# Performance work log

Hardware: AMD Instinct MI355X
Metric: run time of the kernel (lower is better)

## Reference

```python
import jax, jax.numpy as jnp
import numpy as np

N_PTS = 2048
NUM_GABOR = 2
IMG_H = 512
IMG_W = 512
CHUNK = 32  # gaussians per scan step
ALPHA_THRESH = 1.0 / 255.0


def setup_inputs() -> dict:
    key = jax.random.key(0)
    ks = jax.random.split(key, 6)
    xyz = jax.random.uniform(ks[0], (N_PTS, 2), dtype=jnp.float32) * jnp.array([IMG_W, IMG_H], jnp.float32)
    cov2d = jax.random.uniform(ks[1], (N_PTS, 3), dtype=jnp.float32)
    features_dc = jax.random.normal(ks[2], (N_PTS, 3), dtype=jnp.float32)
    opacity = jnp.ones((N_PTS, 1), jnp.float32)
    gabor_freqs = (jax.random.uniform(ks[3], (N_PTS * NUM_GABOR, 2), dtype=jnp.float32) - 0.5) * 0.002
    gabor_weights = jax.random.uniform(ks[4], (N_PTS * NUM_GABOR, 1), dtype=jnp.float32) * -5.0
    background = jnp.ones((3,), jnp.float32)
    return dict(xyz=xyz, cov2d=cov2d, features_dc=features_dc, opacity=opacity,
                gabor_freqs=gabor_freqs, gabor_weights=gabor_weights,
                background=background, H=IMG_H, W=IMG_W)


def _render(xyz, cov2d, features_dc, opacity, gabor_freqs, gabor_weights, H, W):
    n = xyz.shape[0]
    g = gabor_freqs.shape[0] // n
    dt = xyz.dtype
    # cov elements with lower bound (SLV=False branch)
    covs = cov2d + jnp.array([0.5, 0.0, 0.5], dt)
    sxx, sxy, syy = covs[:, 0], covs[:, 1], covs[:, 2]
    det = sxx * syy - sxy * sxy
    valid = det > 1e-8
    det_s = jnp.where(valid, det, 1.0)
    conic_a = syy / det_s
    conic_b = -sxy / det_s
    conic_c = sxx / det_s
    # radius from max eigenvalue (for visibility filter / radii output)
    mid = 0.5 * (sxx + syy)
    lam = mid + jnp.sqrt(jnp.maximum(mid * mid - det, 0.1))
    radii = jnp.where(valid, jnp.ceil(3.0 * jnp.sqrt(lam)), 0.0).astype(jnp.int32)

    colors = jax.nn.sigmoid(features_dc)                      # color_norm=True
    freqs = jnp.exp(gabor_freqs).reshape(n, g, 2)             # get_gabor_freqs
    gw = jax.nn.sigmoid(gabor_weights).reshape(n, g)          # get_gabor_weights

    px = (jnp.arange(W, dtype=dt) + 0.5)[None, :]             # (1, W)
    py = (jnp.arange(H, dtype=dt) + 0.5)[:, None]             # (H, 1)

    steps = n // CHUNK
    def chunked(a):
        return a.reshape((steps, CHUNK) + a.shape[1:])

    xs = (chunked(xyz[:, 0]), chunked(xyz[:, 1]),
          chunked(conic_a), chunked(conic_b), chunked(conic_c),
          chunked(opacity[:, 0]), chunked(colors),
          chunked(freqs[:, :, 0]), chunked(freqs[:, :, 1]),
          chunked(gw), chunked(valid))

    def body(acc, args):
        x, y, ca, cb, cc, op, col, fx, fy, w, vm = args
        dx = px[None, :, :] - x[:, None, None]                 # (C,1,W)
        dy = py[None, :, :] - y[:, None, None]                 # (C,H,1)
        sigma = 0.5 * (ca[:, None, None] * dx * dx + cc[:, None, None] * dy * dy) \
                + cb[:, None, None] * (dx * dy)                # (C,H,W)
        alpha = op[:, None, None] * jnp.exp(-sigma)
        alpha = jnp.minimum(alpha, 0.999)
        alpha = jnp.where((alpha < ALPHA_THRESH) | (~vm[:, None, None]), 0.0, alpha)
        # gabor modulation: 1 + sum_k w_k * cos(fx_k*dx + fy_k*dy)
        arg = fx[:, :, None, None] * dx[:, None, :, :] + fy[:, :, None, None] * dy[:, None, :, :]
        mod = 1.0 + jnp.sum(w[:, :, None, None] * jnp.cos(arg), axis=1)  # (C,H,W)
        wgt = alpha * mod
        acc = acc + jnp.einsum('nhw,nc->hwc', wgt, col)
        return acc, None

    out, _ = jax.lax.scan(body, jnp.zeros((H, W, 3), dt), xs)
    img = jnp.clip(out, 0.0, 1.0)                              # (H,W,3)
    render = jnp.transpose(img[None], (0, 3, 1, 2))            # (1,3,H,W)
    return render, radii


def reference(xyz, cov2d, features_dc, opacity, gabor_freqs, gabor_weights, background, H, W):
    render, radii = _render(xyz, cov2d, features_dc, opacity, gabor_freqs, gabor_weights, H, W)
    visibility = radii > 0
    return render, radii, visibility
```

## Files before the change

### kernel.cpp

```cpp
#include <hip/hip_runtime.h>
#include <math.h>

#define NPTS 2048
#define NG 2
#define IMG_H 512
#define IMG_W 512
#define HW (IMG_H * IMG_W)
#define RENDER_SIZE (3 * HW)
#define S_MAX 5.5412636f

__device__ __forceinline__ float sigmoidf_(float x) {
    return 1.0f / (1.0f + expf(-x));
}

__global__ void init_kernel(const float* __restrict__ cov2d, float* __restrict__ out) {
    int i = blockIdx.x * blockDim.x + threadIdx.x;
    if (i < RENDER_SIZE) out[i] = 0.0f;
    if (i < NPTS) {
        float sxx = cov2d[i * 3 + 0] + 0.5f;
        float sxy = cov2d[i * 3 + 1];
        float syy = cov2d[i * 3 + 2] + 0.5f;
        float det = __fsub_rn(__fmul_rn(sxx, syy), __fmul_rn(sxy, sxy));
        bool valid = det > 1e-8f;
        float mid = __fmul_rn(0.5f, __fadd_rn(sxx, syy));
        float t = __fsub_rn(__fmul_rn(mid, mid), det);
        t = fmaxf(t, 0.1f);
        float lam = __fadd_rn(mid, sqrtf(t));
        float r = valid ? ceilf(__fmul_rn(3.0f, sqrtf(lam))) : 0.0f;
        out[RENDER_SIZE + i] = r;
        out[RENDER_SIZE + NPTS + i] = (r > 0.0f) ? 1.0f : 0.0f;
    }
}

__global__ __launch_bounds__(64) void splat_kernel(
    const float* __restrict__ xyz, const float* __restrict__ cov2d,
    const float* __restrict__ fdc, const float* __restrict__ opac,
    const float* __restrict__ gfreq, const float* __restrict__ gwts,
    float* __restrict__ out)
{
    int p = blockIdx.x;
    float sxx = cov2d[p * 3 + 0] + 0.5f;
    float sxy = cov2d[p * 3 + 1];
    float syy = cov2d[p * 3 + 2] + 0.5f;
    float det = sxx * syy - sxy * sxy;
    if (!(det > 1e-8f)) return;

    float inv = 1.0f / det;
    float ca = syy * inv;
    float cb = -sxy * inv;
    float cc = sxx * inv;

    float xn = xyz[p * 2 + 0];
    float yn = xyz[p * 2 + 1];
    float op = opac[p];

    float c0 = sigmoidf_(fdc[p * 3 + 0]);
    float c1 = sigmoidf_(fdc[p * 3 + 1]);
    float c2 = sigmoidf_(fdc[p * 3 + 2]);

    float fx0 = expf(gfreq[(p * NG + 0) * 2 + 0]);
    float fy0 = expf(gfreq[(p * NG + 0) * 2 + 1]);
    float fx1 = expf(gfreq[(p * NG + 1) * 2 + 0]);
    float fy1 = expf(gfreq[(p * NG + 1) * 2 + 1]);
    float w0 = sigmoidf_(gwts[p * NG + 0]);
    float w1 = sigmoidf_(gwts[p * NG + 1]);

    float dxm = sqrtf(2.0f * S_MAX * sxx) + 0.01f;
    float dym = sqrtf(2.0f * S_MAX * syy) + 0.01f;
    int x0 = max(0, (int)ceilf(xn - dxm - 0.5f));
    int x1 = min(IMG_W - 1, (int)floorf(xn + dxm - 0.5f));
    int y0 = max(0, (int)ceilf(yn - dym - 0.5f));
    int y1 = min(IMG_H - 1, (int)floorf(yn + dym - 0.5f));
    int bw = x1 - x0 + 1;
    int bh = y1 - y0 + 1;
    if (bw <= 0 || bh <= 0) return;
    int area = bw * bh;

    for (int idx = threadIdx.x; idx < area; idx += 64) {
        int ix = x0 + idx % bw;
        int iy = y0 + idx / bw;
        float dx = (ix + 0.5f) - xn;
        float dy = (iy + 0.5f) - yn;
        float sigma = 0.5f * (ca * dx * dx + cc * dy * dy) + cb * (dx * dy);
        float alpha = op * expf(-sigma);
        alpha = fminf(alpha, 0.999f);
        if (alpha < (1.0f / 255.0f)) continue;
        float mod = 1.0f + w0 * cosf(fx0 * dx + fy0 * dy)
                         + w1 * cosf(fx1 * dx + fy1 * dy);
        float wgt = alpha * mod;
        int pix = iy * IMG_W + ix;
        atomicAdd(&out[pix],          wgt * c0);
        atomicAdd(&out[HW + pix],     wgt * c1);
        atomicAdd(&out[2 * HW + pix], wgt * c2);
    }
}

__global__ void clamp_kernel(float* __restrict__ out) {
    int i = blockIdx.x * blockDim.x + threadIdx.x;
    if (i < RENDER_SIZE) {
        float v = out[i];
        out[i] = fminf(fmaxf(v, 0.0f), 1.0f);
    }
}

extern "C" void kernel_launch(void* const* d_in, const int* in_sizes, int n_in,
                              void* d_out, int out_size, void* d_ws, size_t ws_size,
                              hipStream_t stream) {
    const float* xyz   = (const float*)d_in[0];
    const float* cov2d = (const float*)d_in[1];
    const float* fdc   = (const float*)d_in[2];
    const float* opac  = (const float*)d_in[3];
    const float* gfreq = (const float*)d_in[4];
    const float* gwts  = (const float*)d_in[5];
    float* out = (float*)d_out;

    int blocks = (RENDER_SIZE + 255) / 256;
    init_kernel<<<blocks, 256, 0, stream>>>(cov2d, out);
    splat_kernel<<<NPTS, 64, 0, stream>>>(xyz, cov2d, fdc, opac, gfreq, gwts, out);
    clamp_kernel<<<blocks, 256, 0, stream>>>(out);
}
```

Baseline: 79.59 us.

## Replace atomic splatting with per-tile gather rendering in a single fused kernel

Replaces the three-kernel pipeline (zero/radii init, per-gaussian atomic scatter, clamp) with one kernel that assigns each 32x8 pixel tile to a block. Each block culls all gaussians against its tile's bounds, stages the parameters of the overlapping ones in shared memory, accumulates color per pixel in registers, then clamps and writes once. The radii and visibility outputs are computed by two threads per block. This removes global atomics, the separate zero and clamp passes, and the extra launches. In exchange every block scans the full gaussian list, and tiles with more than 128 overlapping gaussians would silently drop the excess.

Result: no change. 79.11 us (-0.6%).

```diff
diff --git a/kernel.cpp b/kernel.cpp
--- a/kernel.cpp
+++ b/kernel.cpp
@@ -9,14 +9,43 @@
 #define RENDER_SIZE (3 * HW)
 #define S_MAX 5.5412636f
 
+#define TILE_W 32
+#define TILE_H 8
+#define TILES_X (IMG_W / TILE_W)
+#define TILES_Y (IMG_H / TILE_H)
+#define NTILES (TILES_X * TILES_Y)
+#define NTHREADS 256
+#define CAP 128
+
 __device__ __forceinline__ float sigmoidf_(float x) {
     return 1.0f / (1.0f + expf(-x));
 }
 
-__global__ void init_kernel(const float* __restrict__ cov2d, float* __restrict__ out) {
-    int i = blockIdx.x * blockDim.x + threadIdx.x;
-    if (i < RENDER_SIZE) out[i] = 0.0f;
-    if (i < NPTS) {
+struct PParam {
+    float xn, yn, ca, cb, cc, op;
+    float c0, c1, c2;
+    float fx0, fy0, fx1, fy1, w0, w1, pad;
+};
+
+__global__ __launch_bounds__(NTHREADS) void render_kernel(
+    const float* __restrict__ xyz, const float* __restrict__ cov2d,
+    const float* __restrict__ fdc, const float* __restrict__ opac,
+    const float* __restrict__ gfreq, const float* __restrict__ gwts,
+    float* __restrict__ out)
+{
+    __shared__ int s_cnt;
+    __shared__ int s_idx[CAP];
+    __shared__ PParam s_prm[CAP];
+
+    const int tid = threadIdx.x;
+    const int tile = blockIdx.x;
+    const int x0 = (tile % TILES_X) * TILE_W;
+    const int y0 = (tile / TILES_X) * TILE_H;
+
+    if (tid == 0) s_cnt = 0;
+
+    if (tid < 2) {
+        int i = tile * 2 + tid;
         float sxx = cov2d[i * 3 + 0] + 0.5f;
         float sxy = cov2d[i * 3 + 1];
         float syy = cov2d[i * 3 + 2] + 0.5f;
@@ -30,77 +59,79 @@
         out[RENDER_SIZE + i] = r;
         out[RENDER_SIZE + NPTS + i] = (r > 0.0f) ? 1.0f : 0.0f;
     }
-}
+    __syncthreads();
 
-__global__ __launch_bounds__(64) void splat_kernel(
-    const float* __restrict__ xyz, const float* __restrict__ cov2d,
-    const float* __restrict__ fdc, const float* __restrict__ opac,
-    const float* __restrict__ gfreq, const float* __restrict__ gwts,
-    float* __restrict__ out)
-{
-    int p = blockIdx.x;
-    float sxx = cov2d[p * 3 + 0] + 0.5f;
-    float sxy = cov2d[p * 3 + 1];
-    float syy = cov2d[p * 3 + 2] + 0.5f;
-    float det = sxx * syy - sxy * sxy;
-    if (!(det > 1e-8f)) return;
+    const float txlo = x0 + 0.5f, txhi = x0 + (TILE_W - 1) + 0.5f;
+    const float tylo = y0 + 0.5f, tyhi = y0 + (TILE_H - 1) + 0.5f;
+    for (int p = tid; p < NPTS; p += NTHREADS) {
+        float2 c = ((const float2*)xyz)[p];
+        float sxx = cov2d[p * 3 + 0] + 0.5f;
+        float sxy = cov2d[p * 3 + 1];
+        float syy = cov2d[p * 3 + 2] + 0.5f;
+        float det = sxx * syy - sxy * sxy;
+        if (!(det > 1e-8f)) continue;
+        float dxn = fmaxf(0.0f, fmaxf(txlo - c.x, c.x - txhi));
+        float dyn = fmaxf(0.0f, fmaxf(tylo - c.y, c.y - tyhi));
+        if (dxn * dxn <= 2.0f * S_MAX * sxx + 0.25f &&
+            dyn * dyn <= 2.0f * S_MAX * syy + 0.25f) {
+            int slot = atomicAdd(&s_cnt, 1);
+            if (slot < CAP) s_idx[slot] = p;
+        }
+    }
+    __syncthreads();
+    const int n = min(s_cnt, CAP);
 
-    float inv = 1.0f / det;
-    float ca = syy * inv;
-    float cb = -sxy * inv;
-    float cc = sxx * inv;
+    for (int i = tid; i < n; i += NTHREADS) {
+        int p = s_idx[i];
+        float sxx = cov2d[p * 3 + 0] + 0.5f;
+        float sxy = cov2d[p * 3 + 1];
+        float syy = cov2d[p * 3 + 2] + 0.5f;
+        float inv = 1.0f / (sxx * syy - sxy * sxy);
+        PParam q;
+        q.xn = xyz[p * 2 + 0];
+        q.yn = xyz[p * 2 + 1];
+        q.ca = syy * inv;
+        q.cb = -sxy * inv;
+        q.cc = sxx * inv;
+        q.op = opac[p];
+        q.c0 = sigmoidf_(fdc[p * 3 + 0]);
+        q.c1 = sigmoidf_(fdc[p * 3 + 1]);
+        q.c2 = sigmoidf_(fdc[p * 3 + 2]);
+        q.fx0 = expf(gfreq[(p * NG + 0) * 2 + 0]);
+        q.fy0 = expf(gfreq[(p * NG + 0) * 2 + 1]);
+        q.fx1 = expf(gfreq[(p * NG + 1) * 2 + 0]);
+        q.fy1 = expf(gfreq[(p * NG + 1) * 2 + 1]);
+        q.w0 = sigmoidf_(gwts[p * NG + 0]);
+        q.w1 = sigmoidf_(gwts[p * NG + 1]);
+        q.pad = 0.0f;
+        s_prm[i] = q;
+    }
+    __syncthreads();
 
-    float xn = xyz[p * 2 + 0];
-    float yn = xyz[p * 2 + 1];
-    float op = opac[p];
-
-    float c0 = sigmoidf_(fdc[p * 3 + 0]);
-    float c1 = sigmoidf_(fdc[p * 3 + 1]);
-    float c2 = sigmoidf_(fdc[p * 3 + 2]);
-
-    float fx0 = expf(gfreq[(p * NG + 0) * 2 + 0]);
-    float fy0 = expf(gfreq[(p * NG + 0) * 2 + 1]);
-    float fx1 = expf(gfreq[(p * NG + 1) * 2 + 0]);
-    float fy1 = expf(gfreq[(p * NG + 1) * 2 + 1]);
-    float w0 = sigmoidf_(gwts[p * NG + 0]);
-    float w1 = sigmoidf_(gwts[p * NG + 1]);
-
-    float dxm = sqrtf(2.0f * S_MAX * sxx) + 0.01f;
-    float dym = sqrtf(2.0f * S_MAX * syy) + 0.01f;
-    int x0 = max(0, (int)ceilf(xn - dxm - 0.5f));
-    int x1 = min(IMG_W - 1, (int)floorf(xn + dxm - 0.5f));
-    int y0 = max(0, (int)ceilf(yn - dym - 0.5f));
-    int y1 = min(IMG_H - 1, (int)floorf(yn + dym - 0.5f));
-    int bw = x1 - x0 + 1;
-    int bh = y1 - y0 + 1;
-    if (bw <= 0 || bh <= 0) return;
-    int area = bw * bh;
-
-    for (int idx = threadIdx.x; idx < area; idx += 64) {
-        int ix = x0 + idx % bw;
-        int iy = y0 + idx / bw;
-        float dx = (ix + 0.5f) - xn;
-        float dy = (iy + 0.5f) - yn;
-        float sigma = 0.5f * (ca * dx * dx + cc * dy * dy) + cb * (dx * dy);
-        float alpha = op * expf(-sigma);
+    const int tx = tid % TILE_W;
+    const int ty = tid / TILE_W;
+    const float px = x0 + tx + 0.5f;
+    const float py = y0 + ty + 0.5f;
+    float accr = 0.0f, accg = 0.0f, accb = 0.0f;
+    for (int i = 0; i < n; ++i) {
+        PParam q = s_prm[i];
+        float dx = px - q.xn;
+        float dy = py - q.yn;
+        float sigma = 0.5f * (q.ca * dx * dx + q.cc * dy * dy) + q.cb * (dx * dy);
+        float alpha = q.op * expf(-sigma);
         alpha = fminf(alpha, 0.999f);
         if (alpha < (1.0f / 255.0f)) continue;
-        float mod = 1.0f + w0 * cosf(fx0 * dx + fy0 * dy)
-                         + w1 * cosf(fx1 * dx + fy1 * dy);
+        float mod = 1.0f + q.w0 * cosf(q.fx0 * dx + q.fy0 * dy)
+                         + q.w1 * cosf(q.fx1 * dx + q.fy1 * dy);
         float wgt = alpha * mod;
-        int pix = iy * IMG_W + ix;
-        atomicAdd(&out[pix],          wgt * c0);
-        atomicAdd(&out[HW + pix],     wgt * c1);
-        atomicAdd(&out[2 * HW + pix], wgt * c2);
+        accr += wgt * q.c0;
+        accg += wgt * q.c1;
+        accb += wgt * q.c2;
     }
-}
-
-__global__ void clamp_kernel(float* __restrict__ out) {
-    int i = blockIdx.x * blockDim.x + threadIdx.x;
-    if (i < RENDER_SIZE) {
-        float v = out[i];
-        out[i] = fminf(fmaxf(v, 0.0f), 1.0f);
-    }
+    const int pix = (y0 + ty) * IMG_W + (x0 + tx);
+    out[pix]          = fminf(fmaxf(accr, 0.0f), 1.0f);
+    out[HW + pix]     = fminf(fmaxf(accg, 0.0f), 1.0f);
+    out[2 * HW + pix] = fminf(fmaxf(accb, 0.0f), 1.0f);
 }
 
 extern "C" void kernel_launch(void* const* d_in, const int* in_sizes, int n_in,
@@ -114,8 +145,6 @@
     const float* gwts  = (const float*)d_in[5];
     float* out = (float*)d_out;
 
-    int blocks = (RENDER_SIZE + 255) / 256;
-    init_kernel<<<blocks, 256, 0, stream>>>(cov2d, out);
-    splat_kernel<<<NPTS, 64, 0, stream>>>(xyz, cov2d, fdc, opac, gfreq, gwts, out);
-    clamp_kernel<<<blocks, 256, 0, stream>>>(out);
+    render_kernel<<<NTILES, NTHREADS, 0, stream>>>(
+        xyz, cov2d, fdc, opac, gfreq, gwts, out);
 }
```
